# Kernel optimization log

Hardware: AMD Instinct MI355X
Metric: run time of the kernel (lower is better)

The kernel has to match this reference:

```python
import jax, jax.numpy as jnp
import numpy as np

H, NH, HD = 1024, 16, 64
B, T, S = 2, 1024, 3
NOISE, STEP, TEMP, NSTEPS = 0.1, 0.01, 1.0, 5
LN_EPS = 1e-5


def setup_inputs() -> dict:
    key = jax.random.key(0)
    ks = jax.random.split(key, 9)
    return {
        "queries": jax.random.normal(ks[0], (B, NH, T, HD), jnp.float32),
        "keys": jax.random.normal(ks[1], (B, NH, T, HD), jnp.float32),
        "values": jax.random.normal(ks[2], (B, NH, T, HD), jnp.float32),
        "hidden_states": jax.random.normal(ks[3], (B, T, H), jnp.float32),
        "W1": jax.random.normal(ks[4], (H, H), jnp.float32) * 0.02,
        "b1": jnp.zeros((H,), jnp.float32),
        "ln_g": jnp.ones((H,), jnp.float32),
        "ln_b": jnp.zeros((H,), jnp.float32),
        "W2": jax.random.normal(ks[5], (H, H), jnp.float32) * 0.02,
        "b2": jnp.zeros((H,), jnp.float32),
        "hyp_noise": jax.random.normal(ks[6], (S, B, NH, T, HD), jnp.float32),
        "ref_noise": jax.random.normal(ks[7], (S, NSTEPS - 1, B, NH, T, HD), jnp.float32),
    }


def _attention_energy(q, k, v):
    # q: [S,B,H,T,D]; k,v: [B,H,T,D] -> energy [S,B]
    scores = jnp.einsum('sbhtd,bhud->sbhtu', q, k) / jnp.sqrt(jnp.float32(q.shape[-1]))
    attn = jax.nn.softmax(scores, axis=-1)
    out = jnp.einsum('sbhtu,bhud->sbhtd', attn, v)
    out_mag = jnp.linalg.norm(out, axis=-1).mean(axis=(2, 3))          # [S,B]
    entropy = -(attn * jnp.log(attn + 1e-8)).sum(axis=-1).mean(axis=(2, 3))
    align = (q * k[None]).sum(axis=-1).mean(axis=(2, 3))
    return out_mag - 0.1 * entropy - 0.05 * align


def reference(queries, keys, values, hidden_states, W1, b1, ln_g, ln_b, W2, b2,
              hyp_noise, ref_noise):
    # query_predictor: Linear -> LayerNorm -> ReLU -> Linear
    x = hidden_states @ W1.T + b1
    mu = x.mean(axis=-1, keepdims=True)
    var = ((x - mu) ** 2).mean(axis=-1, keepdims=True)
    x = (x - mu) / jnp.sqrt(var + LN_EPS) * ln_g + ln_b
    x = jax.nn.relu(x)
    ctx = x @ W2.T + b2                                   # [B,T,H]
    ctx = ctx.reshape(B, T, NH, HD).transpose(0, 2, 1, 3) # [B,NH,T,HD]

    # exploration hypotheses, refined jointly over the sample axis
    q = queries[None] + hyp_noise * NOISE                 # [S,B,NH,T,HD]
    for step in range(NSTEPS):
        q = q - STEP * (q - ctx[None])                    # PCN prediction-error update
        if step < NSTEPS - 1:
            q = q + ref_noise[:, step] * 0.01

    energies = _attention_energy(q, keys, values)         # [S,B]
    probs = jax.nn.softmax(-energies / TEMP, axis=0)      # [S,B]
    selected = jnp.einsum('sb,sbhtd->bhtd', probs, q)     # softmax-weighted mix
    return selected, keys, values
```

## Files before the change

kernel.cpp:

```cpp
#include <hip/hip_runtime.h>
#include <hip/hip_bf16.h>
#include <math.h>

#define NB 2
#define NHH 16
#define TT 1024
#define HDD 64
#define NSS 3
#define HH 1024
#define MMR 2048

typedef float f4 __attribute__((ext_vector_type(4)));
typedef short bf16x8 __attribute__((ext_vector_type(8)));
typedef unsigned short u16;
typedef u16 u16x4 __attribute__((ext_vector_type(4)));

__device__ inline u16 f2bf(float f) {
    union { float f; unsigned u; } v; v.f = f;
    unsigned r = (v.u + 0x7FFFu + ((v.u >> 16) & 1u)) >> 16;
    return (u16)r;
}
__device__ inline float bf2f(u16 u) {
    union { unsigned u; float f; } v; v.u = ((unsigned)u) << 16;
    return v.f;
}

__device__ inline float red16sum(float v) {
    v += __shfl_xor(v, 1);
    v += __shfl_xor(v, 2);
    v += __shfl_xor(v, 4);
    v += __shfl_xor(v, 8);
    return v;
}
__device__ inline float red64sum(float v) {
    v += __shfl_xor(v, 1);
    v += __shfl_xor(v, 2);
    v += __shfl_xor(v, 4);
    v += __shfl_xor(v, 8);
    v += __shfl_xor(v, 16);
    v += __shfl_xor(v, 32);
    return v;
}

__global__ __launch_bounds__(256) void k_cvt4(const float* __restrict__ s0, u16* __restrict__ d0,
                                              const float* __restrict__ s1, u16* __restrict__ d1,
                                              const float* __restrict__ s2, u16* __restrict__ d2,
                                              const float* __restrict__ s3, u16* __restrict__ d3) {
    int b = blockIdx.x;
    const float* s; u16* d; int base;
    if (b < 2048)      { s = s0; d = d0; base = 0; }
    else if (b < 3072) { s = s1; d = d1; base = 2048; }
    else if (b < 4096) { s = s2; d = d2; base = 3072; }
    else               { s = s3; d = d3; base = 4096; }
    int i = (b - base) * 256 + threadIdx.x;
    f4 v = ((const f4*)s)[i];
    u16x4 o;
    o[0] = f2bf(v[0]); o[1] = f2bf(v[1]); o[2] = f2bf(v[2]); o[3] = f2bf(v[3]);
    ((u16x4*)d)[i] = o;
}

__global__ __launch_bounds__(256) void k_vtrans(const float* __restrict__ V,
                                                u16* __restrict__ Vt) {
    __shared__ float tile[64][65];
    int bh = blockIdx.y, t0 = blockIdx.x * 64;
    int r = threadIdx.x >> 2, c0 = (threadIdx.x & 3) * 16;
    const float* vp = V + ((size_t)bh * TT + t0) * HDD;
#pragma unroll
    for (int j = 0; j < 16; j += 4) {
        f4 v = *(const f4*)(vp + r * HDD + c0 + j);
        tile[r][c0 + j + 0] = v[0]; tile[r][c0 + j + 1] = v[1];
        tile[r][c0 + j + 2] = v[2]; tile[r][c0 + j + 3] = v[3];
    }
    __syncthreads();
    int d = threadIdx.x >> 2, x0 = (threadIdx.x & 3) * 16;
    u16* op = Vt + ((size_t)bh * HDD + d) * TT + t0 + x0;
#pragma unroll
    for (int j = 0; j < 16; j += 4) {
        u16x4 o;
        o[0] = f2bf(tile[x0 + j + 0][d]); o[1] = f2bf(tile[x0 + j + 1][d]);
        o[2] = f2bf(tile[x0 + j + 2][d]); o[3] = f2bf(tile[x0 + j + 3][d]);
        *(u16x4*)(op + j) = o;
    }
}

template <int EPI>
__global__ __launch_bounds__(256) void k_gemm_bt(const u16* __restrict__ A,
                                                 const u16* __restrict__ Bm,
                                                 const float* __restrict__ bias,
                                                 float* __restrict__ out) {
    const int K = 1024, N = 1024;
    int w = threadIdx.x >> 6, l = threadIdx.x & 63, lr = l & 15, lg = l >> 4;
    int m0 = blockIdx.y * 64 + w * 16;
    int n0 = blockIdx.x * 64;
    const u16* ap = A + (size_t)(m0 + lr) * K + lg * 8;
    const u16* bp = Bm + (size_t)(n0 + lr) * K + lg * 8;
    f4 z4 = {0.f, 0.f, 0.f, 0.f};
    f4 acc[4] = {z4, z4, z4, z4};
#pragma unroll 2
    for (int kk = 0; kk < K; kk += 32) {
        bf16x8 a  = *(const bf16x8*)(ap + kk);
        bf16x8 b0 = *(const bf16x8*)(bp + kk);
        bf16x8 b1 = *(const bf16x8*)(bp + 16 * K + kk);
        bf16x8 b2 = *(const bf16x8*)(bp + 32 * K + kk);
        bf16x8 b3 = *(const bf16x8*)(bp + 48 * K + kk);
        acc[0] = __builtin_amdgcn_mfma_f32_16x16x32_bf16(a, b0, acc[0], 0, 0, 0);
        acc[1] = __builtin_amdgcn_mfma_f32_16x16x32_bf16(a, b1, acc[1], 0, 0, 0);
        acc[2] = __builtin_amdgcn_mfma_f32_16x16x32_bf16(a, b2, acc[2], 0, 0, 0);
        acc[3] = __builtin_amdgcn_mfma_f32_16x16x32_bf16(a, b3, acc[3], 0, 0, 0);
    }
#pragma unroll
    for (int cf = 0; cf < 4; ++cf) {
        int col = n0 + cf * 16 + lr;
        float bs = bias[col];
#pragma unroll
        for (int r = 0; r < 4; ++r) {
            int row = m0 + lg * 4 + r;
            float v = acc[cf][r] + bs;
            if (EPI == 0) {
                out[(size_t)row * N + col] = v;
            } else {
                int b = row >> 10, t = row & 1023, nh = col >> 6, hd = col & 63;
                out[(((size_t)(b * NHH + nh)) * TT + t) * HDD + hd] = v;
            }
        }
    }
}

__global__ __launch_bounds__(256) void k_lnrelu(const float* __restrict__ X,
                                                const float* __restrict__ g,
                                                const float* __restrict__ bta,
                                                u16* __restrict__ xr) {
    int row = blockIdx.x;
    f4 v = ((const f4*)(X + (size_t)row * HH))[threadIdx.x];
    float s = v[0] + v[1] + v[2] + v[3];
    float s2 = v[0] * v[0] + v[1] * v[1] + v[2] * v[2] + v[3] * v[3];
    s = red64sum(s);
    s2 = red64sum(s2);
    __shared__ float red[8];
    int w = threadIdx.x >> 6, l = threadIdx.x & 63;
    if (l == 0) { red[w] = s; red[w + 4] = s2; }
    __syncthreads();
    float S1 = red[0] + red[1] + red[2] + red[3];
    float S2 = red[4] + red[5] + red[6] + red[7];
    float mu = S1 * (1.0f / 1024.0f);
    float var = S2 * (1.0f / 1024.0f) - mu * mu;
    float rstd = rsqrtf(var + 1e-5f);
    f4 gv = ((const f4*)g)[threadIdx.x];
    f4 bv = ((const f4*)bta)[threadIdx.x];
    u16x4 o;
#pragma unroll
    for (int j = 0; j < 4; ++j) {
        float y = (v[j] - mu) * rstd * gv[j] + bv[j];
        y = fmaxf(y, 0.f);
        o[j] = f2bf(y);
    }
    ((u16x4*)(xr + (size_t)row * HH))[threadIdx.x] = o;
}

__global__ __launch_bounds__(256) void k_qform(const float* __restrict__ que,
                                               const float* __restrict__ hyp,
                                               const float* __restrict__ rn,
                                               const float* __restrict__ ctx,
                                               float* __restrict__ q) {
    int i = blockIdx.x * 256 + threadIdx.x;
    const float A5 = 0.9509900499f;
    const float CC = 1.0f - A5;
    const float CH = 0.1f * A5;
    const float C0 = 0.0096059601f, C1 = 0.0097029900f, C2 = 0.0098010000f, C3 = 0.0099f;
    const int NQ4 = (NB * NHH * TT * HDD) / 4;
    f4 qv = ((const f4*)que)[i];
    f4 cv = ((const f4*)ctx)[i];
    f4 base = A5 * qv + CC * cv;
#pragma unroll
    for (int s = 0; s < 3; ++s) {
        f4 h  = ((const f4*)hyp)[s * NQ4 + i];
        f4 r0 = ((const f4*)rn)[(s * 4 + 0) * NQ4 + i];
        f4 r1 = ((const f4*)rn)[(s * 4 + 1) * NQ4 + i];
        f4 r2 = ((const f4*)rn)[(s * 4 + 2) * NQ4 + i];
        f4 r3 = ((const f4*)rn)[(s * 4 + 3) * NQ4 + i];
        f4 o = base + CH * h + C0 * r0 + C1 * r1 + C2 * r2 + C3 * r3;
        ((f4*)q)[s * NQ4 + i] = o;
    }
}

__global__ __launch_bounds__(256, 3) void k_attn(const float* __restrict__ q,
                                                 const u16* __restrict__ Kb,
                                                 const u16* __restrict__ Vt,
                                                 float* __restrict__ part) {
    int bi = blockIdx.x;
    int qt2 = bi & 7, h = (bi >> 3) & 15, sb = bi >> 7;
    int b = sb & 1;
    int bh = b * NHH + h;
    int w = threadIdx.x >> 6, l = threadIdx.x & 63, lr = l & 15, lg = l >> 4;
    int t0 = qt2 * 128;
    f4 z4 = {0.f, 0.f, 0.f, 0.f};

    __shared__ u16 Ks[4096];
    __shared__ u16 Vs[4096];
    __shared__ u16 plds[8][1024];

    bf16x8 aq[2][2];
#pragma unroll
    for (int qr = 0; qr < 2; ++qr) {
        const float* qp = q + (((size_t)(sb * NHH + h)) * TT + t0 + w * 32 + qr * 16 + lr) * HDD + lg * 8;
        f4 v0 = *(const f4*)(qp);
        f4 v1 = *(const f4*)(qp + 4);
        f4 v2 = *(const f4*)(qp + 32);
        f4 v3 = *(const f4*)(qp + 36);
#pragma unroll
        for (int j = 0; j < 4; ++j) {
            aq[qr][0][j]     = (short)f2bf(v0[j] * 0.125f);
            aq[qr][0][4 + j] = (short)f2bf(v1[j] * 0.125f);
            aq[qr][1][j]     = (short)f2bf(v2[j] * 0.125f);
            aq[qr][1][4 + j] = (short)f2bf(v3[j] * 0.125f);
        }
    }

    const u16* kbase = Kb + (size_t)bh * TT * HDD;
    const u16* vbase = Vt + (size_t)bh * HDD * TT;
    int u0 = threadIdx.x, u1 = threadIdx.x + 256;
    const u16* kg0 = kbase + u0 * 8;
    const u16* kg1 = kbase + u1 * 8;
    const u16* vg0 = vbase + (size_t)(u0 >> 3) * TT + (u0 & 7) * 8;
    const u16* vg1 = vbase + (size_t)(u1 >> 3) * TT + (u1 & 7) * 8;
    int ko0 = (u0 >> 3) * 128 + (((u0 & 7) ^ ((u0 >> 3) & 7)) << 4);
    int ko1 = (u1 >> 3) * 128 + (((u1 & 7) ^ ((u1 >> 3) & 7)) << 4);
    char* KsB = (char*)Ks;
    char* VsB = (char*)Vs;

    int4 kr0 = *(const int4*)(kg0);
    int4 kr1 = *(const int4*)(kg1);
    int4 vr0 = *(const int4*)(vg0);
    int4 vr1 = *(const int4*)(vg1);

    f4 acco[2][4] = {{z4, z4, z4, z4}, {z4, z4, z4, z4}};
    float zrow[2][4] = {{0.f, 0.f, 0.f, 0.f}, {0.f, 0.f, 0.f, 0.f}};
    float wrow[2][4] = {{0.f, 0.f, 0.f, 0.f}, {0.f, 0.f, 0.f, 0.f}};

    for (int kt = 0; kt < 16; ++kt) {
        __syncthreads();
        *(int4*)(KsB + ko0) = kr0;
        *(int4*)(KsB + ko1) = kr1;
        *(int4*)(VsB + ko0) = vr0;
        *(int4*)(VsB + ko1) = vr1;
        if (kt < 15) {
            kr0 = *(const int4*)(kg0 + (kt + 1) * 4096);
            kr1 = *(const int4*)(kg1 + (kt + 1) * 4096);
            vr0 = *(const int4*)(vg0 + (kt + 1) * 64);
            vr1 = *(const int4*)(vg1 + (kt + 1) * 64);
        }
        __syncthreads();

        f4 sc[2][4];
#pragma unroll
        for (int cf = 0; cf < 4; ++cf) {
            int row = cf * 16 + lr, rs = row & 7;
            bf16x8 bk0 = *(const bf16x8*)(KsB + row * 128 + ((lg ^ rs) << 4));
            bf16x8 bk1 = *(const bf16x8*)(KsB + row * 128 + (((4 + lg) ^ rs) << 4));
            f4 t0a = __builtin_amdgcn_mfma_f32_16x16x32_bf16(aq[0][0], bk0, z4, 0, 0, 0);
            sc[0][cf] = __builtin_amdgcn_mfma_f32_16x16x32_bf16(aq[0][1], bk1, t0a, 0, 0, 0);
            f4 t1a = __builtin_amdgcn_mfma_f32_16x16x32_bf16(aq[1][0], bk0, z4, 0, 0, 0);
            sc[1][cf] = __builtin_amdgcn_mfma_f32_16x16x32_bf16(aq[1][1], bk1, t1a, 0, 0, 0);
        }

#pragma unroll
        for (int qr = 0; qr < 2; ++qr) {
            u16* pl = &plds[w * 2 + qr][0];
#pragma unroll
            for (int cf = 0; cf < 4; ++cf) {
#pragma unroll
                for (int r = 0; r < 4; ++r) {
                    float sv = sc[qr][cf][r];
                    float pe = __expf(sv);
                    zrow[qr][r] += pe;
                    wrow[qr][r] = fmaf(pe, sv, wrow[qr][r]);
                    int prow = lg * 4 + r;
                    pl[(prow * 64 + cf * 16 + lr) ^ ((prow & 7) << 3)] = f2bf(pe);
                }
            }
        }
        bf16x8 pa[2][2];
#pragma unroll
        for (int qr = 0; qr < 2; ++qr) {
            const u16* pl = &plds[w * 2 + qr][0];
            pa[qr][0] = *(const bf16x8*)&pl[(lr * 64 + lg * 8) ^ ((lr & 7) << 3)];
            pa[qr][1] = *(const bf16x8*)&pl[(lr * 64 + 32 + lg * 8) ^ ((lr & 7) << 3)];
        }
#pragma unroll
        for (int cf = 0; cf < 4; ++cf) {
            int row = cf * 16 + lr, rs = row & 7;
            bf16x8 bv0 = *(const bf16x8*)(VsB + row * 128 + ((lg ^ rs) << 4));
            bf16x8 bv1 = *(const bf16x8*)(VsB + row * 128 + (((4 + lg) ^ rs) << 4));
            acco[0][cf] = __builtin_amdgcn_mfma_f32_16x16x32_bf16(pa[0][0], bv0, acco[0][cf], 0, 0, 0);
            acco[0][cf] = __builtin_amdgcn_mfma_f32_16x16x32_bf16(pa[0][1], bv1, acco[0][cf], 0, 0, 0);
            acco[1][cf] = __builtin_amdgcn_mfma_f32_16x16x32_bf16(pa[1][0], bv0, acco[1][cf], 0, 0, 0);
            acco[1][cf] = __builtin_amdgcn_mfma_f32_16x16x32_bf16(pa[1][1], bv1, acco[1][cf], 0, 0, 0);
        }
    }

    float magw = 0.f, entw = 0.f;
#pragma unroll
    for (int qr = 0; qr < 2; ++qr) {
#pragma unroll
        for (int r = 0; r < 4; ++r) {
            float zz = red16sum(zrow[qr][r]);
            float ww = red16sum(wrow[qr][r]);
            float ssq = acco[qr][0][r] * acco[qr][0][r] + acco[qr][1][r] * acco[qr][1][r] +
                        acco[qr][2][r] * acco[qr][2][r] + acco[qr][3][r] * acco[qr][3][r];
            ssq = red16sum(ssq);
            float inv = 1.0f / zz;
            magw += sqrtf(ssq) * inv;
            entw += __logf(zz) - ww * inv;
        }
    }
    magw += __shfl_xor(magw, 16); magw += __shfl_xor(magw, 32);
    entw += __shfl_xor(entw, 16); entw += __shfl_xor(entw, 32);

    int arow = threadIdx.x >> 1, ah = (threadIdx.x & 1) * 32;
    const float* qa = q + (((size_t)(sb * NHH + h)) * TT + t0 + arow) * HDD + ah;
    const u16* ka = Kb + (((size_t)bh) * TT + t0 + arow) * HDD + ah;
    float al = 0.f;
#pragma unroll
    for (int j = 0; j < 32; j += 4) {
        f4 qv4 = *(const f4*)(qa + j);
        al += qv4[0] * bf2f(ka[j]) + qv4[1] * bf2f(ka[j + 1]) +
              qv4[2] * bf2f(ka[j + 2]) + qv4[3] * bf2f(ka[j + 3]);
    }
    al = red64sum(al);

    __shared__ float red[4][3];
    if (l == 0) { red[w][0] = magw; red[w][1] = entw; red[w][2] = al; }
    __syncthreads();
    if (threadIdx.x == 0) {
        part[bi * 3 + 0] = red[0][0] + red[1][0] + red[2][0] + red[3][0];
        part[bi * 3 + 1] = red[0][1] + red[1][1] + red[2][1] + red[3][1];
        part[bi * 3 + 2] = red[0][2] + red[1][2] + red[2][2] + red[3][2];
    }
}

__global__ void k_finalize(const float* __restrict__ part, float* __restrict__ probs) {
    int w = threadIdx.x >> 6, l = threadIdx.x & 63;
    __shared__ float eng[6];
    if (w < 6) {
        float a0 = 0.f, a1 = 0.f, a2 = 0.f;
        for (int i = l; i < 128; i += 64) {
            const float* pp = part + (size_t)(w * 128 + i) * 3;
            a0 += pp[0]; a1 += pp[1]; a2 += pp[2];
        }
        a0 = red64sum(a0); a1 = red64sum(a1); a2 = red64sum(a2);
        if (l == 0) {
            const float inv = 1.0f / 16384.0f;
            eng[w] = a0 * inv - 0.1f * (a1 * inv) - 0.05f * (a2 * inv);
        }
    }
    __syncthreads();
    if (threadIdx.x < 2) {
        int b = threadIdx.x;
        float e0 = -eng[0 + b], e1 = -eng[2 + b], e2 = -eng[4 + b];
        float mx = fmaxf(e0, fmaxf(e1, e2));
        float x0 = __expf(e0 - mx), x1 = __expf(e1 - mx), x2 = __expf(e2 - mx);
        float inv = 1.0f / (x0 + x1 + x2);
        probs[0 + b] = x0 * inv;
        probs[2 + b] = x1 * inv;
        probs[4 + b] = x2 * inv;
    }
}

__global__ __launch_bounds__(256) void k_select(const float* __restrict__ q,
                                                const float* __restrict__ probs,
                                                const float* __restrict__ keys,
                                                const float* __restrict__ values,
                                                float* __restrict__ out) {
    const int NQ4 = 524288;
    int blk = blockIdx.x;
    if (blk < 2048) {
        int i = blk * 256 + threadIdx.x;
        int b = i >> 18;
        float p0 = probs[0 + b], p1 = probs[2 + b], p2 = probs[4 + b];
        f4 v = p0 * ((const f4*)q)[i] + p1 * ((const f4*)q)[NQ4 + i] +
               p2 * ((const f4*)q)[2 * NQ4 + i];
        ((f4*)out)[i] = v;
    } else if (blk < 4096) {
        int i = (blk - 2048) * 256 + threadIdx.x;
        ((f4*)out)[NQ4 + i] = ((const f4*)keys)[i];
    } else {
        int i = (blk - 4096) * 256 + threadIdx.x;
        ((f4*)out)[2 * NQ4 + i] = ((const f4*)values)[i];
    }
}

extern "C" void kernel_launch(void* const* d_in, const int* in_sizes, int n_in,
                              void* d_out, int out_size, void* d_ws, size_t ws_size,
                              hipStream_t stream) {
    const float* queries = (const float*)d_in[0];
    const float* keys    = (const float*)d_in[1];
    const float* values  = (const float*)d_in[2];
    const float* hs      = (const float*)d_in[3];
    const float* W1      = (const float*)d_in[4];
    const float* b1      = (const float*)d_in[5];
    const float* ln_g    = (const float*)d_in[6];
    const float* ln_b    = (const float*)d_in[7];
    const float* W2      = (const float*)d_in[8];
    const float* b2      = (const float*)d_in[9];
    const float* hyp     = (const float*)d_in[10];
    const float* rn      = (const float*)d_in[11];
    float* out = (float*)d_out;
    char* ws = (char*)d_ws;

    const size_t MB = 1024ull * 1024ull;
    float* qq   = (float*)(ws);
    u16*   hs_b = (u16*)(ws + 0 * MB);
    u16*   w1_b = (u16*)(ws + 4 * MB);
    u16*   w2_b = (u16*)(ws + 6 * MB);
    float* X    = (float*)(ws + 8 * MB);
    u16*   xr   = (u16*)(ws + 16 * MB);
    float* ctx  = (float*)(ws + 24 * MB);
    u16*   k_b  = (u16*)(ws + 32 * MB);
    u16*   vt_b = (u16*)(ws + 36 * MB);
    float* part = (float*)(ws + 40 * MB);
    float* probs= (float*)(ws + 40 * MB + 65536);

    k_cvt4<<<6144, 256, 0, stream>>>(hs, hs_b, W1, w1_b, W2, w2_b, keys, k_b);
    k_vtrans<<<dim3(16, 32), 256, 0, stream>>>(values, vt_b);

    k_gemm_bt<0><<<dim3(16, 32), 256, 0, stream>>>(hs_b, w1_b, b1, X);
    k_lnrelu<<<2048, 256, 0, stream>>>(X, ln_g, ln_b, xr);
    k_gemm_bt<1><<<dim3(16, 32), 256, 0, stream>>>(xr, w2_b, b2, ctx);

    k_qform<<<2048, 256, 0, stream>>>(queries, hyp, rn, ctx, qq);
    k_attn<<<768, 256, 0, stream>>>(qq, k_b, vt_b, part);
    k_finalize<<<1, 384, 0, stream>>>(part, probs);
    k_select<<<6144, 256, 0, stream>>>(qq, probs, keys, values, out);
}
```

Measured before the change: 183.7 us.

## Store refined hypotheses as bf16 and fuse key/value output copies into conversion kernels

The refined query hypotheses are now written once as bf16 instead of fp32. The attention kernel loads them directly as MFMA operands, and the select kernel reads them at half the width. The 1/8 score scale moves from the queries onto the bf16 keys, and the alignment term is multiplied back by 8. The pass-through copies of keys and values into the output are folded into the existing conversion and transpose kernels, and the noise streams in qform use nontemporal loads. Together these cut global memory traffic, at the cost of bf16 rounding in the returned selected tensor and in the alignment energy.

```diff
diff --git a/kernel.cpp b/kernel.cpp
--- a/kernel.cpp
+++ b/kernel.cpp
@@ -45,13 +45,23 @@
 __global__ __launch_bounds__(256) void k_cvt4(const float* __restrict__ s0, u16* __restrict__ d0,
                                               const float* __restrict__ s1, u16* __restrict__ d1,
                                               const float* __restrict__ s2, u16* __restrict__ d2,
-                                              const float* __restrict__ s3, u16* __restrict__ d3) {
+                                              const float* __restrict__ s3, u16* __restrict__ d3,
+                                              float* __restrict__ outk) {
     int b = blockIdx.x;
+    if (b >= 4096) {
+        int i = (b - 4096) * 256 + threadIdx.x;
+        f4 v = ((const f4*)s3)[i];
+        ((f4*)outk)[i] = v;
+        u16x4 o;
+        o[0] = f2bf(v[0] * 0.125f); o[1] = f2bf(v[1] * 0.125f);
+        o[2] = f2bf(v[2] * 0.125f); o[3] = f2bf(v[3] * 0.125f);
+        ((u16x4*)d3)[i] = o;
+        return;
+    }
     const float* s; u16* d; int base;
     if (b < 2048)      { s = s0; d = d0; base = 0; }
     else if (b < 3072) { s = s1; d = d1; base = 2048; }
-    else if (b < 4096) { s = s2; d = d2; base = 3072; }
-    else               { s = s3; d = d3; base = 4096; }
+    else               { s = s2; d = d2; base = 3072; }
     int i = (b - base) * 256 + threadIdx.x;
     f4 v = ((const f4*)s)[i];
     u16x4 o;
@@ -60,7 +70,8 @@
 }
 
 __global__ __launch_bounds__(256) void k_vtrans(const float* __restrict__ V,
-                                                u16* __restrict__ Vt) {
+                                                u16* __restrict__ Vt,
+                                                float* __restrict__ outv) {
     __shared__ float tile[64][65];
     int bh = blockIdx.y, t0 = blockIdx.x * 64;
     int r = threadIdx.x >> 2, c0 = (threadIdx.x & 3) * 16;
@@ -70,6 +81,7 @@
         f4 v = *(const f4*)(vp + r * HDD + c0 + j);
         tile[r][c0 + j + 0] = v[0]; tile[r][c0 + j + 1] = v[1];
         tile[r][c0 + j + 2] = v[2]; tile[r][c0 + j + 3] = v[3];
+        *(f4*)(outv + ((size_t)bh * TT + t0 + r) * HDD + c0 + j) = v;
     }
     __syncthreads();
     int d = threadIdx.x >> 2, x0 = (threadIdx.x & 3) * 16;
@@ -161,29 +173,38 @@
                                                const float* __restrict__ hyp,
                                                const float* __restrict__ rn,
                                                const float* __restrict__ ctx,
-                                               float* __restrict__ q) {
-    int i = blockIdx.x * 256 + threadIdx.x;
-    const float A5 = 0.9509900499f;
-    const float CC = 1.0f - A5;
-    const float CH = 0.1f * A5;
+                                               u16* __restrict__ qq) {
+    const int NQ4 = 524288;
+    int bx = blockIdx.x;
+    int s = bx >> 10;
+    int i = ((bx & 1023) * 256 + threadIdx.x) * 2;
+    const float A5 = 0.9509900499f, CC = 1.0f - A5, CH = 0.1f * A5;
     const float C0 = 0.0096059601f, C1 = 0.0097029900f, C2 = 0.0098010000f, C3 = 0.0099f;
-    const int NQ4 = (NB * NHH * TT * HDD) / 4;
-    f4 qv = ((const f4*)que)[i];
-    f4 cv = ((const f4*)ctx)[i];
-    f4 base = A5 * qv + CC * cv;
-#pragma unroll
-    for (int s = 0; s < 3; ++s) {
-        f4 h  = ((const f4*)hyp)[s * NQ4 + i];
-        f4 r0 = ((const f4*)rn)[(s * 4 + 0) * NQ4 + i];
-        f4 r1 = ((const f4*)rn)[(s * 4 + 1) * NQ4 + i];
-        f4 r2 = ((const f4*)rn)[(s * 4 + 2) * NQ4 + i];
-        f4 r3 = ((const f4*)rn)[(s * 4 + 3) * NQ4 + i];
-        f4 o = base + CH * h + C0 * r0 + C1 * r1 + C2 * r2 + C3 * r3;
-        ((f4*)q)[s * NQ4 + i] = o;
-    }
-}
-
-__global__ __launch_bounds__(256, 3) void k_attn(const float* __restrict__ q,
+    const f4* qp  = (const f4*)que;
+    const f4* cp  = (const f4*)ctx;
+    const f4* hp  = (const f4*)hyp + (size_t)s * NQ4;
+    const f4* r0p = (const f4*)rn + (size_t)(s * 4 + 0) * NQ4;
+    const f4* r1p = (const f4*)rn + (size_t)(s * 4 + 1) * NQ4;
+    const f4* r2p = (const f4*)rn + (size_t)(s * 4 + 2) * NQ4;
+    const f4* r3p = (const f4*)rn + (size_t)(s * 4 + 3) * NQ4;
+    u16 ob[8];
+#pragma unroll
+    for (int j = 0; j < 2; ++j) {
+        f4 qv = qp[i + j];
+        f4 cv = cp[i + j];
+        f4 h  = __builtin_nontemporal_load(hp + i + j);
+        f4 r0 = __builtin_nontemporal_load(r0p + i + j);
+        f4 r1 = __builtin_nontemporal_load(r1p + i + j);
+        f4 r2 = __builtin_nontemporal_load(r2p + i + j);
+        f4 r3 = __builtin_nontemporal_load(r3p + i + j);
+        f4 v = A5 * qv + CC * cv + CH * h + C0 * r0 + C1 * r1 + C2 * r2 + C3 * r3;
+        ob[j * 4 + 0] = f2bf(v[0]); ob[j * 4 + 1] = f2bf(v[1]);
+        ob[j * 4 + 2] = f2bf(v[2]); ob[j * 4 + 3] = f2bf(v[3]);
+    }
+    *(int4*)(qq + (size_t)s * 4 * NQ4 + (size_t)i * 4) = *(const int4*)ob;
+}
+
+__global__ __launch_bounds__(256, 3) void k_attn(const u16* __restrict__ qq,
                                                  const u16* __restrict__ Kb,
                                                  const u16* __restrict__ Vt,
                                                  float* __restrict__ part) {
@@ -202,18 +223,9 @@
     bf16x8 aq[2][2];
 #pragma unroll
     for (int qr = 0; qr < 2; ++qr) {
-        const float* qp = q + (((size_t)(sb * NHH + h)) * TT + t0 + w * 32 + qr * 16 + lr) * HDD + lg * 8;
-        f4 v0 = *(const f4*)(qp);
-        f4 v1 = *(const f4*)(qp + 4);
-        f4 v2 = *(const f4*)(qp + 32);
-        f4 v3 = *(const f4*)(qp + 36);
-#pragma unroll
-        for (int j = 0; j < 4; ++j) {
-            aq[qr][0][j]     = (short)f2bf(v0[j] * 0.125f);
-            aq[qr][0][4 + j] = (short)f2bf(v1[j] * 0.125f);
-            aq[qr][1][j]     = (short)f2bf(v2[j] * 0.125f);
-            aq[qr][1][4 + j] = (short)f2bf(v3[j] * 0.125f);
-        }
+        const u16* qrow = qq + (((size_t)(sb * NHH + h)) * TT + t0 + w * 32 + qr * 16 + lr) * HDD;
+        aq[qr][0] = *(const bf16x8*)(qrow + lg * 8);
+        aq[qr][1] = *(const bf16x8*)(qrow + 32 + lg * 8);
     }
 
     const u16* kbase = Kb + (size_t)bh * TT * HDD;
@@ -317,16 +329,17 @@
     entw += __shfl_xor(entw, 16); entw += __shfl_xor(entw, 32);
 
     int arow = threadIdx.x >> 1, ah = (threadIdx.x & 1) * 32;
-    const float* qa = q + (((size_t)(sb * NHH + h)) * TT + t0 + arow) * HDD + ah;
+    const u16* qa = qq + (((size_t)(sb * NHH + h)) * TT + t0 + arow) * HDD + ah;
     const u16* ka = Kb + (((size_t)bh) * TT + t0 + arow) * HDD + ah;
     float al = 0.f;
 #pragma unroll
     for (int j = 0; j < 32; j += 4) {
-        f4 qv4 = *(const f4*)(qa + j);
-        al += qv4[0] * bf2f(ka[j]) + qv4[1] * bf2f(ka[j + 1]) +
-              qv4[2] * bf2f(ka[j + 2]) + qv4[3] * bf2f(ka[j + 3]);
-    }
-    al = red64sum(al);
+        u16x4 qv4 = *(const u16x4*)(qa + j);
+        u16x4 kv4 = *(const u16x4*)(ka + j);
+        al += bf2f(qv4[0]) * bf2f(kv4[0]) + bf2f(qv4[1]) * bf2f(kv4[1]) +
+              bf2f(qv4[2]) * bf2f(kv4[2]) + bf2f(qv4[3]) * bf2f(kv4[3]);
+    }
+    al = red64sum(al) * 8.0f;
 
     __shared__ float red[4][3];
     if (l == 0) { red[w][0] = magw; red[w][1] = entw; red[w][2] = al; }
@@ -366,27 +379,21 @@
     }
 }
 
-__global__ __launch_bounds__(256) void k_select(const float* __restrict__ q,
+__global__ __launch_bounds__(256) void k_select(const u16* __restrict__ qq,
                                                 const float* __restrict__ probs,
-                                                const float* __restrict__ keys,
-                                                const float* __restrict__ values,
                                                 float* __restrict__ out) {
     const int NQ4 = 524288;
-    int blk = blockIdx.x;
-    if (blk < 2048) {
-        int i = blk * 256 + threadIdx.x;
-        int b = i >> 18;
-        float p0 = probs[0 + b], p1 = probs[2 + b], p2 = probs[4 + b];
-        f4 v = p0 * ((const f4*)q)[i] + p1 * ((const f4*)q)[NQ4 + i] +
-               p2 * ((const f4*)q)[2 * NQ4 + i];
-        ((f4*)out)[i] = v;
-    } else if (blk < 4096) {
-        int i = (blk - 2048) * 256 + threadIdx.x;
-        ((f4*)out)[NQ4 + i] = ((const f4*)keys)[i];
-    } else {
-        int i = (blk - 4096) * 256 + threadIdx.x;
-        ((f4*)out)[2 * NQ4 + i] = ((const f4*)values)[i];
-    }
+    int i = blockIdx.x * 256 + threadIdx.x;
+    int b = i >> 18;
+    float p0 = probs[0 + b], p1 = probs[2 + b], p2 = probs[4 + b];
+    u16x4 a0 = ((const u16x4*)qq)[i];
+    u16x4 a1 = ((const u16x4*)qq)[NQ4 + i];
+    u16x4 a2 = ((const u16x4*)qq)[2 * NQ4 + i];
+    f4 v;
+#pragma unroll
+    for (int j = 0; j < 4; ++j)
+        v[j] = p0 * bf2f(a0[j]) + p1 * bf2f(a1[j]) + p2 * bf2f(a2[j]);
+    ((f4*)out)[i] = v;
 }
 
 extern "C" void kernel_launch(void* const* d_in, const int* in_sizes, int n_in,
@@ -408,7 +415,7 @@
     char* ws = (char*)d_ws;
 
     const size_t MB = 1024ull * 1024ull;
-    float* qq   = (float*)(ws);
+    u16*   qq16 = (u16*)(ws);
     u16*   hs_b = (u16*)(ws + 0 * MB);
     u16*   w1_b = (u16*)(ws + 4 * MB);
     u16*   w2_b = (u16*)(ws + 6 * MB);
@@ -420,15 +427,16 @@
     float* part = (float*)(ws + 40 * MB);
     float* probs= (float*)(ws + 40 * MB + 65536);
 
-    k_cvt4<<<6144, 256, 0, stream>>>(hs, hs_b, W1, w1_b, W2, w2_b, keys, k_b);
-    k_vtrans<<<dim3(16, 32), 256, 0, stream>>>(values, vt_b);
+    k_cvt4<<<6144, 256, 0, stream>>>(hs, hs_b, W1, w1_b, W2, w2_b, keys, k_b,
+                                     out + 2097152);
+    k_vtrans<<<dim3(16, 32), 256, 0, stream>>>(values, vt_b, out + 4194304);
 
     k_gemm_bt<0><<<dim3(16, 32), 256, 0, stream>>>(hs_b, w1_b, b1, X);
     k_lnrelu<<<2048, 256, 0, stream>>>(X, ln_g, ln_b, xr);
     k_gemm_bt<1><<<dim3(16, 32), 256, 0, stream>>>(xr, w2_b, b2, ctx);
 
-    k_qform<<<2048, 256, 0, stream>>>(queries, hyp, rn, ctx, qq);
-    k_attn<<<768, 256, 0, stream>>>(qq, k_b, vt_b, part);
+    k_qform<<<3072, 256, 0, stream>>>(queries, hyp, rn, ctx, qq16);
+    k_attn<<<768, 256, 0, stream>>>(qq16, k_b, vt_b, part);
     k_finalize<<<1, 384, 0, stream>>>(part, probs);
-    k_select<<<6144, 256, 0, stream>>>(qq, probs, keys, values, out);
-}
+    k_select<<<2048, 256, 0, stream>>>(qq16, probs, out);
+}
```

Measured after the change: 179.2 us. -2.4%, faster.
